# Kernel tuning notes

Measured on AMD Instinct MI355X. Metric: run time of the kernel, lower is better.

The kernel has to match this reference:

```python
import jax, jax.numpy as jnp
import numpy as np
import math

B, S, C = 4, 2048, 128
H, DK, DV, K = 8, 64, 64, 3


def setup_inputs() -> dict:
    key = jax.random.key(0)
    ks = jax.random.split(key, 12)
    sd = 0.05
    return {
        "x": jax.random.normal(ks[0], (B, S, C), dtype=jnp.float32),
        "length": jax.random.randint(ks[1], (B,), 1, S + 1, dtype=jnp.int32),
        "wq": jax.random.normal(ks[2], (H * DK, C, K), dtype=jnp.float32) * sd,
        "bq": jnp.zeros((H * DK,), dtype=jnp.float32),
        "wk": jax.random.normal(ks[3], (H * DK, C, K), dtype=jnp.float32) * sd,
        "bk": jnp.zeros((H * DK,), dtype=jnp.float32),
        "wv": jax.random.normal(ks[4], (H * DV, C), dtype=jnp.float32) * sd,
        "bv": jnp.zeros((H * DV,), dtype=jnp.float32),
        "w1": jax.random.normal(ks[5], (DV, H * DV), dtype=jnp.float32) * sd,
        "b1": jnp.zeros((DV,), dtype=jnp.float32),
        "w2": jax.random.normal(ks[6], (1, DV), dtype=jnp.float32) * sd,
        "b2": jnp.zeros((1,), dtype=jnp.float32),
    }


def _causal_conv(x, w, b):
    # x: (b,s,c), w: (o,c,k) torch Conv1d layout -> (b,s,o), causal (left) padding
    y = jax.lax.conv_general_dilated(
        x.transpose(0, 2, 1), w, window_strides=(1,), padding=[(K - 1, 0)],
        dimension_numbers=("NCH", "OIH", "NCH"))
    return y.transpose(0, 2, 1) + b


def _split_heads(x, d):
    b, s, _ = x.shape
    return x.reshape(b, s, H, d).transpose(0, 2, 1, 3)  # (b,h,s,d)


def reference(x, length, wq, bq, wk, bk, wv, bv, w1, b1, w2, b2):
    q = _split_heads(_causal_conv(x, wq, bq), DK)            # (b,h,s,dk)
    k = _split_heads(_causal_conv(x, wk, bk), DK)            # (b,h,s,dk)
    v = _split_heads(jax.nn.relu(x @ wv.T + bv), DV)         # (b,h,s,dv)

    attn = jnp.einsum("bhqd,bhkd->bhqk", q, k) / math.sqrt(DK)
    # future mask: additive -1e9 above the diagonal (matches triu * -1e9 + softmax)
    future = jnp.triu(jnp.ones((S, S), dtype=attn.dtype), k=1) * (-1e9)
    score = jax.nn.softmax(attn + future, axis=-1)
    # padding mask: zero query rows >= length[b]
    row_valid = (jnp.arange(S)[None, :] < length[:, None]).astype(score.dtype)
    score = score * row_valid[:, None, :, None]              # (b,h,s,s)

    out1 = jnp.einsum("bhqk,bhkd->bhqd", score, v)           # (b,h,s,dv)
    out2 = out1.transpose(0, 2, 1, 3).reshape(x.shape[0], S, H * DV)
    out3 = jax.nn.relu(out2 @ w1.T + b1) @ w2.T + b2         # (b,s,1)
    return out3, score
```

## Files before the change

### kernel.cpp

```cpp
#include <hip/hip_runtime.h>

#define S_ 2048
#define C_ 128
#define B_ 4
#define H_ 8
#define D_ 64

typedef __attribute__((ext_vector_type(8))) short bf16x8;
typedef __attribute__((ext_vector_type(4))) float f32x4;

__device__ inline unsigned short f2bf(float f) {
    union { float f; unsigned int u; } c; c.f = f;
    unsigned int u = c.u;
    unsigned int r = (u + 0x7FFFu + ((u >> 16) & 1u)) >> 16;
    return (unsigned short)r;
}
__device__ inline float bf2f(unsigned short s) {
    union { unsigned int u; float f; } c; c.u = ((unsigned int)s) << 16;
    return c.f;
}

__global__ __launch_bounds__(256) void prep_kernel(
    const float* __restrict__ x,
    const float* __restrict__ wq, const float* __restrict__ wk,
    const float* __restrict__ wv, const float* __restrict__ w1,
    unsigned short* __restrict__ xh,
    unsigned short* __restrict__ wPackQ, unsigned short* __restrict__ wPackK,
    unsigned short* __restrict__ wPackV, float* __restrict__ w1T4)
{
    int idx = blockIdx.x * 256 + threadIdx.x;
    if (idx < 262144) {
        float4 v = *(const float4*)&x[idx * 4];
        ushort4 o;
        o.x = f2bf(v.x); o.y = f2bf(v.y); o.z = f2bf(v.z); o.w = f2bf(v.w);
        *(ushort4*)&xh[idx * 4] = o;
    } else if (idx < 458752) {
        int i = idx - 262144;
        int t = i >> 16, r = i & 65535;
        int o = r >> 7, c = r & 127;
        wPackQ[i] = f2bf(wq[o * 384 + c * 3 + t]);
    } else if (idx < 655360) {
        int i = idx - 458752;
        int t = i >> 16, r = i & 65535;
        int o = r >> 7, c = r & 127;
        wPackK[i] = f2bf(wk[o * 384 + c * 3 + t]);
    } else if (idx < 720896) {
        int i = idx - 655360;
        wPackV[i] = f2bf(wv[i]);
    } else if (idx < 753664) {
        int i = idx - 720896;
        int jj = i & 3, d = (i >> 2) & 63, jb = i >> 8;
        w1T4[i] = w1[d * 512 + jb * 4 + jj];
    }
}

__global__ __launch_bounds__(256) void qkv_kernel(
    const unsigned short* __restrict__ xh,
    const unsigned short* __restrict__ wPackQ, const unsigned short* __restrict__ wPackK,
    const unsigned short* __restrict__ wPackV,
    const float* __restrict__ bq, const float* __restrict__ bk,
    const float* __restrict__ bv,
    unsigned short* __restrict__ Qh, unsigned short* __restrict__ Kh,
    unsigned short* __restrict__ VhT)
{
    __shared__ __align__(16) short xs[130 * 136];
    __shared__ __align__(16) short ws[64 * 136];

    int s0 = blockIdx.x * 128;
    int h = blockIdx.y;
    int b = blockIdx.z;
    int bh = b * H_ + h;
    int tid = threadIdx.x;
    int w = tid >> 6;
    int lane = tid & 63;
    int col = lane & 15;
    int quad = lane >> 4;

    for (int i = tid; i < 2080; i += 256) {
        int row = i >> 4, c8 = (i & 15) << 3;
        int s = s0 - 2 + row;
        uint4 v = {0u, 0u, 0u, 0u};
        if (s >= 0) v = *(const uint4*)&xh[((long)b * S_ + s) * C_ + c8];
        *(uint4*)&xs[row * 136 + c8] = v;
    }

    for (int sec = 0; sec < 3; sec++) {
        const unsigned short* wsel = (sec == 0) ? wPackQ : (sec == 1) ? wPackK : wPackV;
        int tlo = (sec == 2) ? 2 : 0;

        f32x4 acc[2][4];
        #pragma unroll
        for (int rt = 0; rt < 2; rt++)
            #pragma unroll
            for (int nt = 0; nt < 4; nt++) acc[rt][nt] = (f32x4){0.f, 0.f, 0.f, 0.f};

        for (int t = tlo; t < 3; t++) {
            if (!(sec == 0 && t == 0)) __syncthreads();
            long wbase = (sec == 2) ? ((long)h * 8192)
                                    : ((long)t * 65536 + (long)h * 8192);
            for (int i = tid; i < 1024; i += 256) {
                int row = i >> 4, c8 = (i & 15) << 3;
                *(uint4*)&ws[row * 136 + c8] = *(const uint4*)&wsel[wbase + row * 128 + c8];
            }
            __syncthreads();

            #pragma unroll
            for (int kc = 0; kc < 4; kc++) {
                int ko = kc * 32 + quad * 8;
                bf16x8 a0 = *(const bf16x8*)&xs[(w * 32 + col + t) * 136 + ko];
                bf16x8 a1 = *(const bf16x8*)&xs[(w * 32 + 16 + col + t) * 136 + ko];
                #pragma unroll
                for (int nt = 0; nt < 4; nt++) {
                    bf16x8 bfr = *(const bf16x8*)&ws[(nt * 16 + col) * 136 + ko];
                    acc[0][nt] = __builtin_amdgcn_mfma_f32_16x16x32_bf16(a0, bfr, acc[0][nt], 0, 0, 0);
                    acc[1][nt] = __builtin_amdgcn_mfma_f32_16x16x32_bf16(a1, bfr, acc[1][nt], 0, 0, 0);
                }
            }
        }

        if (sec == 0) {
            #pragma unroll
            for (int nt = 0; nt < 4; nt++) {
                float bias = bq[h * 64 + nt * 16 + col];
                #pragma unroll
                for (int rt = 0; rt < 2; rt++)
                    #pragma unroll
                    for (int r = 0; r < 4; r++) {
                        int s = s0 + w * 32 + rt * 16 + quad * 4 + r;
                        Qh[((long)bh * S_ + s) * D_ + nt * 16 + col] =
                            f2bf((acc[rt][nt][r] + bias) * 0.18033688011112042f);
                    }
            }
        } else if (sec == 1) {
            #pragma unroll
            for (int nt = 0; nt < 4; nt++) {
                float bias = bk[h * 64 + nt * 16 + col];
                #pragma unroll
                for (int rt = 0; rt < 2; rt++)
                    #pragma unroll
                    for (int r = 0; r < 4; r++) {
                        int s = s0 + w * 32 + rt * 16 + quad * 4 + r;
                        Kh[((long)bh * S_ + s) * D_ + nt * 16 + col] =
                            f2bf(acc[rt][nt][r] + bias);
                    }
            }
        } else {
            __syncthreads();
            #pragma unroll
            for (int nt = 0; nt < 4; nt++) {
                float bias = bv[h * 64 + nt * 16 + col];
                #pragma unroll
                for (int rt = 0; rt < 2; rt++)
                    #pragma unroll
                    for (int r = 0; r < 4; r++) {
                        int sl = w * 32 + rt * 16 + quad * 4 + r;
                        ws[(nt * 16 + col) * 136 + sl] =
                            (short)f2bf(fmaxf(acc[rt][nt][r] + bias, 0.f));
                    }
            }
            __syncthreads();
            for (int i = tid; i < 1024; i += 256) {
                int row = i >> 4, c8 = (i & 15) << 3;
                *(uint4*)&VhT[((long)bh * D_ + row) * S_ + s0 + c8] =
                    *(const uint4*)&ws[row * 136 + c8];
            }
        }
    }
}

#define PST 78
__global__ __launch_bounds__(256) void attn_kernel(
    const unsigned short* __restrict__ Qh, const unsigned short* __restrict__ Kh,
    const unsigned short* __restrict__ VhT, const int* __restrict__ length,
    float* __restrict__ score, float* __restrict__ out2)
{
    __shared__ __align__(16) short Kbuf[2][2][64 * 72];
    __shared__ __align__(16) short Pfh[64 * PST];

    int idx = blockIdx.x;
    int xcd = idx & 7;
    int slot = idx >> 3;
    int t = slot >> 2;
    int qt = (t < 16) ? (31 - t) : (t - 16);
    int bh = (slot & 3) * 8 + xcd;
    int b = bh >> 3, h = bh & 7;
    int q0 = qt * 64;
    int tid = threadIdx.x;
    int w = tid >> 6;
    int lane = tid & 63;
    int col = lane & 15;
    int quad = lane >> 4;
    int len = length[b];

    const unsigned short* Qb = Qh + (long)bh * S_ * D_;
    const unsigned short* Kb = Kh + (long)bh * S_ * D_;
    const unsigned short* Vtb = VhT + (long)bh * D_ * S_;
    float* scb = score + (long)bh * S_ * S_;

    if (q0 >= len) {
        f32x4 z = (f32x4){0.f, 0.f, 0.f, 0.f};
        for (int kt2 = 0; kt2 < 32; kt2++) {
            #pragma unroll
            for (int it = 0; it < 4; it++) {
                int idx2 = tid + it * 256;
                int rr = idx2 >> 4, cc = idx2 & 15;
                __builtin_nontemporal_store(z,
                    (f32x4*)&scb[(long)(q0 + rr) * S_ + kt2 * 64 + cc * 4]);
            }
        }
        #pragma unroll
        for (int it = 0; it < 4; it++) {
            int idx2 = tid + it * 256;
            int rr = idx2 >> 4, cc = idx2 & 15;
            *(f32x4*)&out2[((long)(b * S_ + q0 + rr)) * 512 + h * 64 + cc * 4] = z;
        }
        return;
    }

    int srow_ = tid >> 2, sc16_ = (tid & 3) * 16;

    int arow = w * 16 + col;
    bf16x8 aq0 = *(const bf16x8*)&Qb[(q0 + arow) * D_ + quad * 8];
    bf16x8 aq1 = *(const bf16x8*)&Qb[(q0 + arow) * D_ + 32 + quad * 8];

    float lrun[4];
    #pragma unroll
    for (int r = 0; r < 4; r++) lrun[r] = 0.f;

    {
        *(uint4*)&Kbuf[0][0][srow_ * 72 + sc16_]     = *(const uint4*)&Kb[srow_ * D_ + sc16_];
        *(uint4*)&Kbuf[0][0][srow_ * 72 + sc16_ + 8] = *(const uint4*)&Kb[srow_ * D_ + sc16_ + 8];
    }
    __syncthreads();

    for (int kt = 0; kt <= qt; kt++) {
        int buf = kt & 1;
        if (kt < qt) {
            *(uint4*)&Kbuf[1 - buf][0][srow_ * 72 + sc16_] =
                *(const uint4*)&Kb[((kt + 1) * 64 + srow_) * D_ + sc16_];
            *(uint4*)&Kbuf[1 - buf][0][srow_ * 72 + sc16_ + 8] =
                *(const uint4*)&Kb[((kt + 1) * 64 + srow_) * D_ + sc16_ + 8];
        }

        f32x4 acc[4];
        #pragma unroll
        for (int n = 0; n < 4; n++) acc[n] = (f32x4){0.f, 0.f, 0.f, 0.f};
        #pragma unroll
        for (int n = 0; n < 4; n++) {
            bf16x8 b0 = *(const bf16x8*)&Kbuf[buf][0][(n * 16 + col) * 72 + quad * 8];
            acc[n] = __builtin_amdgcn_mfma_f32_16x16x32_bf16(aq0, b0, acc[n], 0, 0, 0);
            bf16x8 b1 = *(const bf16x8*)&Kbuf[buf][0][(n * 16 + col) * 72 + 32 + quad * 8];
            acc[n] = __builtin_amdgcn_mfma_f32_16x16x32_bf16(aq1, b1, acc[n], 0, 0, 0);
        }
        if (kt == qt) {
            #pragma unroll
            for (int n = 0; n < 4; n++) {
                int kk = kt * 64 + n * 16 + col;
                #pragma unroll
                for (int r = 0; r < 4; r++) {
                    int q = q0 + w * 16 + quad * 4 + r;
                    if (kk > q) acc[n][r] = -1.0e30f;
                }
            }
        }
        #pragma unroll
        for (int r = 0; r < 4; r++) {
            lrun[r] += exp2f(acc[0][r]) + exp2f(acc[1][r]) +
                       exp2f(acc[2][r]) + exp2f(acc[3][r]);
        }
        __syncthreads();
    }

    #pragma unroll
    for (int off = 1; off < 16; off <<= 1) {
        #pragma unroll
        for (int r = 0; r < 4; r++) lrun[r] += __shfl_xor(lrun[r], off, 64);
    }
    float linv[4];
    #pragma unroll
    for (int r = 0; r < 4; r++) linv[r] = 1.0f / lrun[r];

    f32x4 oacc[4];
    #pragma unroll
    for (int n = 0; n < 4; n++) oacc[n] = (f32x4){0.f, 0.f, 0.f, 0.f};

    int prow = w * 16 + quad * 4;
    int rlo = lane >> 4;
    int c4 = (lane & 15) * 4;

#define STAGE2(HALF, KT) do { \
    *(uint4*)&Kbuf[HALF][0][srow_ * 72 + sc16_] = \
        *(const uint4*)&Kb[((KT) * 64 + srow_) * D_ + sc16_]; \
    *(uint4*)&Kbuf[HALF][0][srow_ * 72 + sc16_ + 8] = \
        *(const uint4*)&Kb[((KT) * 64 + srow_) * D_ + sc16_ + 8]; \
    *(uint4*)&Kbuf[HALF][1][srow_ * 72 + sc16_] = \
        *(const uint4*)&Vtb[srow_ * S_ + (KT) * 64 + sc16_]; \
    *(uint4*)&Kbuf[HALF][1][srow_ * 72 + sc16_ + 8] = \
        *(const uint4*)&Vtb[srow_ * S_ + (KT) * 64 + sc16_ + 8]; \
} while (0)

#define TILE2(HALF, KT) do { \
    f32x4 acc[4]; \
    _Pragma("unroll") \
    for (int n = 0; n < 4; n++) acc[n] = (f32x4){0.f, 0.f, 0.f, 0.f}; \
    _Pragma("unroll") \
    for (int n = 0; n < 4; n++) { \
        bf16x8 b0 = *(const bf16x8*)&Kbuf[HALF][0][(n * 16 + col) * 72 + quad * 8]; \
        acc[n] = __builtin_amdgcn_mfma_f32_16x16x32_bf16(aq0, b0, acc[n], 0, 0, 0); \
        bf16x8 b1 = *(const bf16x8*)&Kbuf[HALF][0][(n * 16 + col) * 72 + 32 + quad * 8]; \
        acc[n] = __builtin_amdgcn_mfma_f32_16x16x32_bf16(aq1, b1, acc[n], 0, 0, 0); \
    } \
    bool diag = ((KT) == qt); \
    _Pragma("unroll") \
    for (int n = 0; n < 4; n++) { \
        int kk = (KT) * 64 + n * 16 + col; \
        _Pragma("unroll") \
        for (int r = 0; r < 4; r++) { \
            int q = q0 + prow + r; \
            float pv = exp2f(acc[n][r]) * linv[r]; \
            if (q >= len || (diag && kk > q)) pv = 0.f; \
            Pfh[(prow + r) * PST + n * 16 + col] = (short)f2bf(pv); \
        } \
    } \
    bf16x8 pa0 = *(const bf16x8*)&Pfh[(w * 16 + col) * PST + quad * 8]; \
    bf16x8 pa1 = *(const bf16x8*)&Pfh[(w * 16 + col) * PST + 32 + quad * 8]; \
    _Pragma("unroll") \
    for (int n = 0; n < 4; n++) { \
        bf16x8 vv0 = *(const bf16x8*)&Kbuf[HALF][1][(n * 16 + col) * 72 + quad * 8]; \
        oacc[n] = __builtin_amdgcn_mfma_f32_16x16x32_bf16(pa0, vv0, oacc[n], 0, 0, 0); \
        bf16x8 vv1 = *(const bf16x8*)&Kbuf[HALF][1][(n * 16 + col) * 72 + 32 + quad * 8]; \
        oacc[n] = __builtin_amdgcn_mfma_f32_16x16x32_bf16(pa1, vv1, oacc[n], 0, 0, 0); \
    } \
    _Pragma("unroll") \
    for (int j = 0; j < 4; j++) { \
        int row = w * 16 + j * 4 + rlo; \
        uint2 pk = *(const uint2*)&Pfh[row * PST + c4]; \
        f32x4 v; \
        v[0] = bf2f((unsigned short)(pk.x & 0xFFFFu)); \
        v[1] = bf2f((unsigned short)(pk.x >> 16)); \
        v[2] = bf2f((unsigned short)(pk.y & 0xFFFFu)); \
        v[3] = bf2f((unsigned short)(pk.y >> 16)); \
        __builtin_nontemporal_store(v, \
            (f32x4*)&scb[(long)(q0 + row) * S_ + (KT) * 64 + c4]); \
    } \
} while (0)

    STAGE2(0, 0);
    __syncthreads();
    {
        int kt = 0;
        while (true) {
            if (kt < qt) STAGE2(1, kt + 1);
            TILE2(0, kt);
            __syncthreads();
            kt++; if (kt > qt) break;
            if (kt < qt) STAGE2(0, kt + 1);
            TILE2(1, kt);
            __syncthreads();
            kt++; if (kt > qt) break;
        }
    }
#undef STAGE2
#undef TILE2

    #pragma unroll
    for (int n = 0; n < 4; n++) {
        #pragma unroll
        for (int r = 0; r < 4; r++) {
            int q = q0 + w * 16 + quad * 4 + r;
            out2[((long)(b * S_ + q)) * 512 + h * 64 + n * 16 + col] = oacc[n][r];
        }
    }

    f32x4 z = (f32x4){0.f, 0.f, 0.f, 0.f};
    for (int kt2 = qt + 1; kt2 < 32; kt2++) {
        #pragma unroll
        for (int it = 0; it < 4; it++) {
            int idx2 = tid + it * 256;
            int rr = idx2 >> 4, cc = idx2 & 15;
            __builtin_nontemporal_store(z,
                (f32x4*)&scb[(long)(q0 + rr) * S_ + kt2 * 64 + cc * 4]);
        }
    }
}

__global__ __launch_bounds__(256) void mlp_kernel(
    const float* __restrict__ out2, const float* __restrict__ w1T4,
    const float* __restrict__ b1, const float* __restrict__ w2,
    const float* __restrict__ b2, float* __restrict__ out3)
{
    __shared__ __align__(16) float xr[2048];
    int sg0 = blockIdx.x * 4;
    int tid = threadIdx.x;
    for (int i = tid; i < 512; i += 256)
        *(f32x4*)&xr[i * 4] = *(const f32x4*)&out2[(long)sg0 * 512 + i * 4];
    __syncthreads();

    int sl = tid >> 6, d = tid & 63;
    float acc = 0.f;
    #pragma unroll 4
    for (int jb = 0; jb < 128; jb++) {
        f32x4 xv = *(const f32x4*)&xr[sl * 512 + jb * 4];
        f32x4 wv = *(const f32x4*)&w1T4[jb * 256 + d * 4];
        acc += xv[0] * wv[0] + xv[1] * wv[1] + xv[2] * wv[2] + xv[3] * wv[3];
    }
    float hval = fmaxf(acc + b1[d], 0.f);
    float p = hval * w2[d];
    #pragma unroll
    for (int off = 32; off > 0; off >>= 1) p += __shfl_xor(p, off, 64);
    if (d == 0) out3[sg0 + sl] = p + b2[0];
}

extern "C" void kernel_launch(void* const* d_in, const int* in_sizes, int n_in,
                              void* d_out, int out_size, void* d_ws, size_t ws_size,
                              hipStream_t stream) {
    const float* x      = (const float*)d_in[0];
    const int*   length = (const int*)  d_in[1];
    const float* wq     = (const float*)d_in[2];
    const float* bq     = (const float*)d_in[3];
    const float* wk     = (const float*)d_in[4];
    const float* bk     = (const float*)d_in[5];
    const float* wv     = (const float*)d_in[6];
    const float* bv     = (const float*)d_in[7];
    const float* w1     = (const float*)d_in[8];
    const float* b1     = (const float*)d_in[9];
    const float* w2     = (const float*)d_in[10];
    const float* b2     = (const float*)d_in[11];

    float* out3  = (float*)d_out;
    float* score = (float*)d_out + 8192;

    float* ws  = (float*)d_ws;
    unsigned short* xh     = (unsigned short*)ws;  ws += 524288;
    unsigned short* wPackQ = (unsigned short*)ws;  ws += 98304;
    unsigned short* wPackK = (unsigned short*)ws;  ws += 98304;
    unsigned short* wPackV = (unsigned short*)ws;  ws += 32768;
    float* w1T4 = ws;  ws += 32768;
    unsigned short* Qh  = (unsigned short*)ws;  ws += 2097152;
    unsigned short* Kh  = (unsigned short*)ws;  ws += 2097152;
    unsigned short* VhT = (unsigned short*)ws;  ws += 2097152;
    float* o2  = ws;  ws += 4194304;

    hipLaunchKernelGGL(prep_kernel, dim3(2944), dim3(256), 0, stream,
                       x, wq, wk, wv, w1, xh, wPackQ, wPackK, wPackV, w1T4);
    hipLaunchKernelGGL(qkv_kernel, dim3(16, 8, 4), dim3(256), 0, stream,
                       xh, wPackQ, wPackK, wPackV, bq, bk, bv, Qh, Kh, VhT);
    hipLaunchKernelGGL(attn_kernel, dim3(1024), dim3(256), 0, stream,
                       Qh, Kh, VhT, length, score, o2);
    hipLaunchKernelGGL(mlp_kernel, dim3(2048), dim3(256), 0, stream,
                       o2, w1T4, b1, w2, b2, out3);
}
```

Baseline: 636.4 us.

## Enlarge attention query tile to 128 rows with two row-tiles per wave

Result: slower. 682.5 us (+7.2%).

```diff
diff --git a/kernel.cpp b/kernel.cpp
--- a/kernel.cpp
+++ b/kernel.cpp
@@ -175,16 +175,20 @@
     float* __restrict__ score, float* __restrict__ out2)
 {
     __shared__ __align__(16) short Kbuf[2][2][64 * 72];
-    __shared__ __align__(16) short Pfh[64 * PST];
+    __shared__ __align__(16) short Pfh[128 * PST];
 
     int idx = blockIdx.x;
     int xcd = idx & 7;
     int slot = idx >> 3;
-    int t = slot >> 2;
-    int qt = (t < 16) ? (31 - t) : (t - 16);
-    int bh = (slot & 3) * 8 + xcd;
-    int b = bh >> 3, h = bh & 7;
-    int q0 = qt * 64;
+    int s0b = slot & 1;
+    int m   = (slot >> 1) & 15;
+    int s5  = slot >> 5;
+    int qt2 = (s0b ^ s5) ? (15 - m) : m;
+    int b   = s5 * 2 + s0b;
+    int h   = xcd;
+    int bh  = b * 8 + h;
+    int q0  = qt2 * 128;
+    int ktmax = 2 * qt2 + 1;
     int tid = threadIdx.x;
     int w = tid >> 6;
     int lane = tid & 63;
@@ -201,7 +205,7 @@
         f32x4 z = (f32x4){0.f, 0.f, 0.f, 0.f};
         for (int kt2 = 0; kt2 < 32; kt2++) {
             #pragma unroll
-            for (int it = 0; it < 4; it++) {
+            for (int it = 0; it < 8; it++) {
                 int idx2 = tid + it * 256;
                 int rr = idx2 >> 4, cc = idx2 & 15;
                 __builtin_nontemporal_store(z,
@@ -209,7 +213,7 @@
             }
         }
         #pragma unroll
-        for (int it = 0; it < 4; it++) {
+        for (int it = 0; it < 8; it++) {
             int idx2 = tid + it * 256;
             int rr = idx2 >> 4, cc = idx2 & 15;
             *(f32x4*)&out2[((long)(b * S_ + q0 + rr)) * 512 + h * 64 + cc * 4] = z;
@@ -219,13 +223,20 @@
 
     int srow_ = tid >> 2, sc16_ = (tid & 3) * 16;
 
-    int arow = w * 16 + col;
-    bf16x8 aq0 = *(const bf16x8*)&Qb[(q0 + arow) * D_ + quad * 8];
-    bf16x8 aq1 = *(const bf16x8*)&Qb[(q0 + arow) * D_ + 32 + quad * 8];
-
-    float lrun[4];
-    #pragma unroll
-    for (int r = 0; r < 4; r++) lrun[r] = 0.f;
+    bf16x8 aq[2][2];
+    {
+        int ar = q0 + w * 32 + col;
+        aq[0][0] = *(const bf16x8*)&Qb[ar * D_ + quad * 8];
+        aq[0][1] = *(const bf16x8*)&Qb[ar * D_ + 32 + quad * 8];
+        aq[1][0] = *(const bf16x8*)&Qb[(ar + 16) * D_ + quad * 8];
+        aq[1][1] = *(const bf16x8*)&Qb[(ar + 16) * D_ + 32 + quad * 8];
+    }
+
+    float lrun[2][4];
+    #pragma unroll
+    for (int rt = 0; rt < 2; rt++)
+        #pragma unroll
+        for (int r = 0; r < 4; r++) lrun[rt][r] = 0.f;
 
     {
         *(uint4*)&Kbuf[0][0][srow_ * 72 + sc16_]     = *(const uint4*)&Kb[srow_ * D_ + sc16_];
@@ -233,58 +244,72 @@
     }
     __syncthreads();
 
-    for (int kt = 0; kt <= qt; kt++) {
+    for (int kt = 0; kt <= ktmax; kt++) {
         int buf = kt & 1;
-        if (kt < qt) {
+        if (kt < ktmax) {
             *(uint4*)&Kbuf[1 - buf][0][srow_ * 72 + sc16_] =
                 *(const uint4*)&Kb[((kt + 1) * 64 + srow_) * D_ + sc16_];
             *(uint4*)&Kbuf[1 - buf][0][srow_ * 72 + sc16_ + 8] =
                 *(const uint4*)&Kb[((kt + 1) * 64 + srow_) * D_ + sc16_ + 8];
         }
 
-        f32x4 acc[4];
-        #pragma unroll
-        for (int n = 0; n < 4; n++) acc[n] = (f32x4){0.f, 0.f, 0.f, 0.f};
+        f32x4 acc[2][4];
+        #pragma unroll
+        for (int rt = 0; rt < 2; rt++)
+            #pragma unroll
+            for (int n = 0; n < 4; n++) acc[rt][n] = (f32x4){0.f, 0.f, 0.f, 0.f};
         #pragma unroll
         for (int n = 0; n < 4; n++) {
             bf16x8 b0 = *(const bf16x8*)&Kbuf[buf][0][(n * 16 + col) * 72 + quad * 8];
-            acc[n] = __builtin_amdgcn_mfma_f32_16x16x32_bf16(aq0, b0, acc[n], 0, 0, 0);
             bf16x8 b1 = *(const bf16x8*)&Kbuf[buf][0][(n * 16 + col) * 72 + 32 + quad * 8];
-            acc[n] = __builtin_amdgcn_mfma_f32_16x16x32_bf16(aq1, b1, acc[n], 0, 0, 0);
-        }
-        if (kt == qt) {
+            #pragma unroll
+            for (int rt = 0; rt < 2; rt++) {
+                acc[rt][n] = __builtin_amdgcn_mfma_f32_16x16x32_bf16(aq[rt][0], b0, acc[rt][n], 0, 0, 0);
+                acc[rt][n] = __builtin_amdgcn_mfma_f32_16x16x32_bf16(aq[rt][1], b1, acc[rt][n], 0, 0, 0);
+            }
+        }
+        if (kt >= 2 * qt2) {
             #pragma unroll
             for (int n = 0; n < 4; n++) {
                 int kk = kt * 64 + n * 16 + col;
                 #pragma unroll
-                for (int r = 0; r < 4; r++) {
-                    int q = q0 + w * 16 + quad * 4 + r;
-                    if (kk > q) acc[n][r] = -1.0e30f;
-                }
-            }
-        }
-        #pragma unroll
-        for (int r = 0; r < 4; r++) {
-            lrun[r] += exp2f(acc[0][r]) + exp2f(acc[1][r]) +
-                       exp2f(acc[2][r]) + exp2f(acc[3][r]);
-        }
+                for (int rt = 0; rt < 2; rt++)
+                    #pragma unroll
+                    for (int r = 0; r < 4; r++) {
+                        int q = q0 + w * 32 + rt * 16 + quad * 4 + r;
+                        if (kk > q) acc[rt][n][r] = -1.0e30f;
+                    }
+            }
+        }
+        #pragma unroll
+        for (int rt = 0; rt < 2; rt++)
+            #pragma unroll
+            for (int r = 0; r < 4; r++) {
+                lrun[rt][r] += exp2f(acc[rt][0][r]) + exp2f(acc[rt][1][r]) +
+                               exp2f(acc[rt][2][r]) + exp2f(acc[rt][3][r]);
+            }
         __syncthreads();
     }
 
     #pragma unroll
     for (int off = 1; off < 16; off <<= 1) {
         #pragma unroll
-        for (int r = 0; r < 4; r++) lrun[r] += __shfl_xor(lrun[r], off, 64);
-    }
-    float linv[4];
-    #pragma unroll
-    for (int r = 0; r < 4; r++) linv[r] = 1.0f / lrun[r];
-
-    f32x4 oacc[4];
-    #pragma unroll
-    for (int n = 0; n < 4; n++) oacc[n] = (f32x4){0.f, 0.f, 0.f, 0.f};
-
-    int prow = w * 16 + quad * 4;
+        for (int rt = 0; rt < 2; rt++)
+            #pragma unroll
+            for (int r = 0; r < 4; r++) lrun[rt][r] += __shfl_xor(lrun[rt][r], off, 64);
+    }
+    float linv[2][4];
+    #pragma unroll
+    for (int rt = 0; rt < 2; rt++)
+        #pragma unroll
+        for (int r = 0; r < 4; r++) linv[rt][r] = 1.0f / lrun[rt][r];
+
+    f32x4 oacc[2][4];
+    #pragma unroll
+    for (int rt = 0; rt < 2; rt++)
+        #pragma unroll
+        for (int n = 0; n < 4; n++) oacc[rt][n] = (f32x4){0.f, 0.f, 0.f, 0.f};
+
     int rlo = lane >> 4;
     int c4 = (lane & 15) * 4;
 
@@ -300,40 +325,53 @@
 } while (0)
 
 #define TILE2(HALF, KT) do { \
-    f32x4 acc[4]; \
+    f32x4 acc[2][4]; \
     _Pragma("unroll") \
-    for (int n = 0; n < 4; n++) acc[n] = (f32x4){0.f, 0.f, 0.f, 0.f}; \
+    for (int rt = 0; rt < 2; rt++) \
+        _Pragma("unroll") \
+        for (int n = 0; n < 4; n++) acc[rt][n] = (f32x4){0.f, 0.f, 0.f, 0.f}; \
     _Pragma("unroll") \
     for (int n = 0; n < 4; n++) { \
         bf16x8 b0 = *(const bf16x8*)&Kbuf[HALF][0][(n * 16 + col) * 72 + quad * 8]; \
-        acc[n] = __builtin_amdgcn_mfma_f32_16x16x32_bf16(aq0, b0, acc[n], 0, 0, 0); \
         bf16x8 b1 = *(const bf16x8*)&Kbuf[HALF][0][(n * 16 + col) * 72 + 32 + quad * 8]; \
-        acc[n] = __builtin_amdgcn_mfma_f32_16x16x32_bf16(aq1, b1, acc[n], 0, 0, 0); \
+        _Pragma("unroll") \
+        for (int rt = 0; rt < 2; rt++) { \
+            acc[rt][n] = __builtin_amdgcn_mfma_f32_16x16x32_bf16(aq[rt][0], b0, acc[rt][n], 0, 0, 0); \
+            acc[rt][n] = __builtin_amdgcn_mfma_f32_16x16x32_bf16(aq[rt][1], b1, acc[rt][n], 0, 0, 0); \
+        } \
     } \
-    bool diag = ((KT) == qt); \
+    bool diag = ((KT) >= 2 * qt2); \
     _Pragma("unroll") \
     for (int n = 0; n < 4; n++) { \
         int kk = (KT) * 64 + n * 16 + col; \
         _Pragma("unroll") \
-        for (int r = 0; r < 4; r++) { \
-            int q = q0 + prow + r; \
-            float pv = exp2f(acc[n][r]) * linv[r]; \
-            if (q >= len || (diag && kk > q)) pv = 0.f; \
-            Pfh[(prow + r) * PST + n * 16 + col] = (short)f2bf(pv); \
-        } \
+        for (int rt = 0; rt < 2; rt++) \
+            _Pragma("unroll") \
+            for (int r = 0; r < 4; r++) { \
+                int q = q0 + w * 32 + rt * 16 + quad * 4 + r; \
+                float pv = exp2f(acc[rt][n][r]) * linv[rt][r]; \
+                if (q >= len || (diag && kk > q)) pv = 0.f; \
+                Pfh[(w * 32 + rt * 16 + quad * 4 + r) * PST + n * 16 + col] = (short)f2bf(pv); \
+            } \
     } \
-    bf16x8 pa0 = *(const bf16x8*)&Pfh[(w * 16 + col) * PST + quad * 8]; \
-    bf16x8 pa1 = *(const bf16x8*)&Pfh[(w * 16 + col) * PST + 32 + quad * 8]; \
+    bf16x8 pa[2][2]; \
+    pa[0][0] = *(const bf16x8*)&Pfh[(w * 32 + col) * PST + quad * 8]; \
+    pa[0][1] = *(const bf16x8*)&Pfh[(w * 32 + col) * PST + 32 + quad * 8]; \
+    pa[1][0] = *(const bf16x8*)&Pfh[(w * 32 + 16 + col) * PST + quad * 8]; \
+    pa[1][1] = *(const bf16x8*)&Pfh[(w * 32 + 16 + col) * PST + 32 + quad * 8]; \
     _Pragma("unroll") \
     for (int n = 0; n < 4; n++) { \
         bf16x8 vv0 = *(const bf16x8*)&Kbuf[HALF][1][(n * 16 + col) * 72 + quad * 8]; \
-        oacc[n] = __builtin_amdgcn_mfma_f32_16x16x32_bf16(pa0, vv0, oacc[n], 0, 0, 0); \
         bf16x8 vv1 = *(const bf16x8*)&Kbuf[HALF][1][(n * 16 + col) * 72 + 32 + quad * 8]; \
-        oacc[n] = __builtin_amdgcn_mfma_f32_16x16x32_bf16(pa1, vv1, oacc[n], 0, 0, 0); \
+        _Pragma("unroll") \
+        for (int rt = 0; rt < 2; rt++) { \
+            oacc[rt][n] = __builtin_amdgcn_mfma_f32_16x16x32_bf16(pa[rt][0], vv0, oacc[rt][n], 0, 0, 0); \
+            oacc[rt][n] = __builtin_amdgcn_mfma_f32_16x16x32_bf16(pa[rt][1], vv1, oacc[rt][n], 0, 0, 0); \
+        } \
     } \
     _Pragma("unroll") \
-    for (int j = 0; j < 4; j++) { \
-        int row = w * 16 + j * 4 + rlo; \
+    for (int j = 0; j < 8; j++) { \
+        int row = w * 32 + j * 4 + rlo; \
         uint2 pk = *(const uint2*)&Pfh[row * PST + c4]; \
         f32x4 v; \
         v[0] = bf2f((unsigned short)(pk.x & 0xFFFFu)); \
@@ -350,32 +388,33 @@
     {
         int kt = 0;
         while (true) {
-            if (kt < qt) STAGE2(1, kt + 1);
+            if (kt < ktmax) STAGE2(1, kt + 1);
             TILE2(0, kt);
             __syncthreads();
-            kt++; if (kt > qt) break;
-            if (kt < qt) STAGE2(0, kt + 1);
+            kt++; if (kt > ktmax) break;
+            if (kt < ktmax) STAGE2(0, kt + 1);
             TILE2(1, kt);
             __syncthreads();
-            kt++; if (kt > qt) break;
+            kt++; if (kt > ktmax) break;
         }
     }
 #undef STAGE2
 #undef TILE2
 
     #pragma unroll
-    for (int n = 0; n < 4; n++) {
-        #pragma unroll
-        for (int r = 0; r < 4; r++) {
-            int q = q0 + w * 16 + quad * 4 + r;
-            out2[((long)(b * S_ + q)) * 512 + h * 64 + n * 16 + col] = oacc[n][r];
-        }
-    }
+    for (int rt = 0; rt < 2; rt++)
+        #pragma unroll
+        for (int n = 0; n < 4; n++)
+            #pragma unroll
+            for (int r = 0; r < 4; r++) {
+                int q = q0 + w * 32 + rt * 16 + quad * 4 + r;
+                out2[((long)(b * S_ + q)) * 512 + h * 64 + n * 16 + col] = oacc[rt][n][r];
+            }
 
     f32x4 z = (f32x4){0.f, 0.f, 0.f, 0.f};
-    for (int kt2 = qt + 1; kt2 < 32; kt2++) {
-        #pragma unroll
-        for (int it = 0; it < 4; it++) {
+    for (int kt2 = ktmax + 1; kt2 < 32; kt2++) {
+        #pragma unroll
+        for (int it = 0; it < 8; it++) {
             int idx2 = tid + it * 256;
             int rr = idx2 >> 4, cc = idx2 & 15;
             __builtin_nontemporal_store(z,
@@ -445,7 +484,7 @@
                        x, wq, wk, wv, w1, xh, wPackQ, wPackK, wPackV, w1T4);
     hipLaunchKernelGGL(qkv_kernel, dim3(16, 8, 4), dim3(256), 0, stream,
                        xh, wPackQ, wPackK, wPackV, bq, bk, bv, Qh, Kh, VhT);
-    hipLaunchKernelGGL(attn_kernel, dim3(1024), dim3(256), 0, stream,
+    hipLaunchKernelGGL(attn_kernel, dim3(512), dim3(256), 0, stream,
                        Qh, Kh, VhT, length, score, o2);
     hipLaunchKernelGGL(mlp_kernel, dim3(2048), dim3(256), 0, stream,
                        o2, w1T4, b1, w2, b2, out3);
```
